# Kernel optimization log

Measured on AMD Instinct MI355X. Metric: run time of the kernel, lower is better.

The kernel has to match this reference:

```python
import jax, jax.numpy as jnp
import numpy as np
from functools import partial

TAU = 2.0       # membrane time constant
V_TH = 1.0      # firing threshold
SLOPE = 10.0    # surrogate sigmoid slope (matches rate_encode's 10*)
T = 10          # time_window
H = 12          # num_heads


def lif_step(v, I):
    """One LIF update: leaky integrate, surrogate spike, multiplicative reset."""
    v = v + (I - v) / TAU
    spk = jax.nn.sigmoid(SLOPE * (v - V_TH))
    v = v * (1.0 - spk)
    return spk, v


def setup_inputs() -> dict:
    key = jax.random.key(0)
    ks = jax.random.split(key, 5)
    B, S, E = 8, 1024, 768
    scale = 1.0 / np.sqrt(E)
    x = jax.random.uniform(ks[0], (B, S, E), dtype=jnp.float32)
    Wq = jax.random.normal(ks[1], (E, E), dtype=jnp.float32) * scale
    Wk = jax.random.normal(ks[2], (E, E), dtype=jnp.float32) * scale
    Wv = jax.random.normal(ks[3], (E, E), dtype=jnp.float32) * scale
    Wo = jax.random.normal(ks[4], (E, E), dtype=jnp.float32) * scale
    zb = jnp.zeros((E,), dtype=jnp.float32)
    return {"x": x, "Wq": Wq, "bq": zb, "Wk": Wk, "bk": zb,
            "Wv": Wv, "bv": zb, "Wo": Wo, "bo": zb}


def reference(x, Wq, bq, Wk, bk, Wv, bv, Wo, bo):
    B, S, E = x.shape
    D = E // H
    # rate encoding probability (x assumed in [0,1] range, clipped)
    p = jnp.clip(x, 0.0, 1.0)  # [B,S,E]

    def step(carry, t):
        vq, vk, vv, Qa, Ka, Va = carry
        inp = jax.nn.sigmoid(SLOPE * (p * T - t))  # [B,S,E] spikes at step t
        qs, vq = lif_step(vq, inp @ Wq.T + bq)
        ks, vk = lif_step(vk, inp @ Wk.T + bk)
        vs, vv = lif_step(vv, inp @ Wv.T + bv)
        return (vq, vk, vv, Qa + qs, Ka + ks, Va + vs), None

    z = jnp.zeros((B, S, E), dtype=x.dtype)
    t_idx = jnp.arange(T, dtype=x.dtype)
    (vq, vk, vv, Q, K, V), _ = jax.lax.scan(step, (z, z, z, z, z, z), t_idx)

    # split heads: [B,S,E] -> [B,H,S,D]
    Qh = Q.reshape(B, S, H, D)
    Kh = K.reshape(B, S, H, D)
    Vh = V.reshape(B, S, H, D)
    scores = jnp.einsum('bqhd,bkhd->bhqk', Qh, Kh) / np.sqrt(D)
    attn = jax.nn.softmax(scores, axis=-1)
    out_h = jnp.einsum('bhqk,bkhd->bqhd', attn, Vh)  # [B,S,H,D]
    out = out_h.reshape(B, S, E)
    # output LIF projection with fresh (zero) state
    out_spk, _ = lif_step(jnp.zeros_like(out), out @ Wo.T + bo)
    return out_spk
```

## Files before the change

### kernel.cpp

```cpp
#include <hip/hip_runtime.h>
#include <math.h>

constexpr int B_ = 8, S_ = 1024, E_ = 768, H_ = 12, D_ = 64, T_ = 10;
constexpr int N_ = B_ * S_;
constexpr int NE_ = N_ * E_;
constexpr int WE_ = E_ * E_;

typedef __attribute__((ext_vector_type(8))) short bf16x8;
typedef __attribute__((ext_vector_type(4))) float f32x4;

#define MFMA16(a,b,c) __builtin_amdgcn_mfma_f32_16x16x32_bf16(a,b,c,0,0,0)

__device__ __forceinline__ float sigm(float z){ return 1.f/(1.f+__expf(-z)); }
__device__ __forceinline__ unsigned short f2bf(float f){
    unsigned int u = __float_as_uint(f);
    u += 0x7FFFu + ((u>>16)&1u);
    return (unsigned short)(u>>16);
}
__device__ __forceinline__ float bf2f(unsigned short h){
    return __uint_as_float(((unsigned int)h)<<16);
}
__device__ __forceinline__ void gl16(const void* g, void* l){
    __builtin_amdgcn_global_load_lds((const __attribute__((address_space(1))) unsigned int*)g,
                                     (__attribute__((address_space(3))) unsigned int*)l, 16, 0, 0);
}

__global__ __launch_bounds__(256) void encode_k(const float* __restrict__ x,
                                                unsigned short* __restrict__ enc){
    const int i = blockIdx.x*256 + threadIdx.x;
    const float4 a = ((const float4*)x)[2*i];
    const float4 b = ((const float4*)x)[2*i+1];
    float p[8] = {a.x,a.y,a.z,a.w,b.x,b.y,b.z,b.w};
#pragma unroll
    for (int e=0;e<8;++e) p[e] = 100.f*fminf(fmaxf(p[e],0.f),1.f);
#pragma unroll
    for (int t=0;t<T_;++t){
        unsigned int w[4];
#pragma unroll
        for (int e=0;e<4;++e){
            unsigned short u0 = f2bf(sigm(p[2*e]   - 10.f*(float)t));
            unsigned short u1 = f2bf(sigm(p[2*e+1] - 10.f*(float)t));
            w[e] = (unsigned int)u0 | ((unsigned int)u1<<16);
        }
        ((uint4*)(enc + (long)t*NE_))[i] = make_uint4(w[0],w[1],w[2],w[3]);
    }
}

__global__ __launch_bounds__(256) void wsplit_k(const float* __restrict__ Wq, const float* __restrict__ Wk,
        const float* __restrict__ Wv, const float* __restrict__ Wo,
        unsigned short* __restrict__ whi, unsigned short* __restrict__ wlo){
    int gi = blockIdx.x*256 + threadIdx.x;
    int z = gi / (WE_/8);
    int r = gi % (WE_/8);
    const float* W = z==0?Wq : z==1?Wk : z==2?Wv : Wo;
    const float4 a = ((const float4*)W)[2*r];
    const float4 b = ((const float4*)W)[2*r+1];
    float f[8]={a.x,a.y,a.z,a.w,b.x,b.y,b.z,b.w};
    unsigned int h[4], l[4];
#pragma unroll
    for (int e=0;e<4;++e){
        unsigned short h0=f2bf(f[2*e]),   l0=f2bf(f[2*e]  -bf2f(h0));
        unsigned short h1=f2bf(f[2*e+1]), l1=f2bf(f[2*e+1]-bf2f(h1));
        h[e] = (unsigned)h0 | ((unsigned)h1<<16);
        l[e] = (unsigned)l0 | ((unsigned)l1<<16);
    }
    ((uint4*)(whi + (long)z*WE_))[r] = make_uint4(h[0],h[1],h[2],h[3]);
    ((uint4*)(wlo + (long)z*WE_))[r] = make_uint4(l[0],l[1],l[2],l[3]);
}

__global__ __launch_bounds__(256,2) void qkv_k(const unsigned short* __restrict__ enc,
        const unsigned short* __restrict__ whi,
        const float* __restrict__ bq, const float* __restrict__ bk, const float* __restrict__ bv,
        float* __restrict__ Qf, float* __restrict__ Kf, float* __restrict__ Vf){
    const int z = blockIdx.z;
    const unsigned short* Wh = whi + (long)z*WE_;
    const float* bias = z==0?bq : z==1?bk : bv;
    float* Out = z==0?Qf : z==1?Kf : Vf;
    const int row0 = blockIdx.x*128, col0 = blockIdx.y*64;

    __shared__ unsigned short Ab[3][128*64];
    __shared__ unsigned short Bh[3][64*64];

    const int tid = threadIdx.x, lane = tid&63, wid = tid>>6;
    const int l15 = lane&15, l4 = lane>>4, l7 = lane&7;
    const int wr = wid>>1, wc = wid&1;

    int aSrc[4], bSrc[2];
#pragma unroll
    for (int s=0;s<4;++s){
        int idx = (wid + s*4)*64 + lane;
        int row = idx>>3, ch = idx&7;
        aSrc[s] = (row0+row)*E_ + ((ch ^ (row&7))<<3);
    }
#pragma unroll
    for (int s=0;s<2;++s){
        int idx = (wid + s*4)*64 + lane;
        int row = idx>>3, ch = idx&7;
        bSrc[s] = (col0+row)*E_ + ((ch ^ (row&7))<<3);
    }

    const int aBase = (wr*64 + l15)*128;
    const int bBase = (wc*32 + l15)*128;
    const int sw[2] = { ((l4^l7)<<4), ((((4+l4))^l7)<<4) };

    f32x4 acc[4][2];
    float vm[4][2][4] = {};
    float qa[4][2][4] = {};
    float bn[2];
#pragma unroll
    for (int n=0;n<2;++n) bn[n] = bias[col0 + wc*32 + n*16 + l15];
    asm volatile("" :: "v"(bn[0]), "v"(bn[1]));

    const f32x4 zero4 = {0.f,0.f,0.f,0.f};

#define STAGE(tt, kk2, slot)                                               \
    do {                                                                   \
        const unsigned short* eb_ = enc + (long)(tt)*NE_ + (kk2)*64;       \
        _Pragma("unroll")                                                  \
        for (int s_=0;s_<4;++s_)                                           \
            gl16(eb_ + aSrc[s_], &Ab[slot][(wid+s_*4)*512]);               \
        _Pragma("unroll")                                                  \
        for (int s_=0;s_<2;++s_)                                           \
            gl16(Wh + bSrc[s_] + (kk2)*64, &Bh[slot][(wid+s_*4)*512]);     \
    } while(0)

    STAGE(0, 0, 0);
    STAGE(0, 1, 1);

    for (int t=0;t<T_;++t){
#pragma unroll
        for (int m=0;m<4;++m)
#pragma unroll
            for (int n=0;n<2;++n) acc[m][n] = zero4;
#pragma unroll
        for (int kt=0;kt<12;++kt){
            const int slotC = kt%3;
            const int slotS = (kt+2)%3;
            if (kt < 10){
                STAGE(t, kt+2, slotS);
                asm volatile("s_waitcnt vmcnt(12)" ::: "memory");
            } else if (t < 9){
                STAGE(t+1, kt-10, slotS);
                asm volatile("s_waitcnt vmcnt(12)" ::: "memory");
            } else if (kt == 10){
                asm volatile("s_waitcnt vmcnt(6)" ::: "memory");
            } else {
                asm volatile("s_waitcnt vmcnt(0)" ::: "memory");
            }
            __builtin_amdgcn_s_barrier();
            __builtin_amdgcn_s_setprio(1);
#pragma unroll
            for (int kk=0;kk<2;++kk){
                bf16x8 af[4], fbh[2];
#pragma unroll
                for (int m=0;m<4;++m)
                    af[m] = *(const bf16x8*)((const char*)&Ab[slotC][0] + aBase + m*2048 + sw[kk]);
#pragma unroll
                for (int n=0;n<2;++n)
                    fbh[n] = *(const bf16x8*)((const char*)&Bh[slotC][0] + bBase + n*2048 + sw[kk]);
#pragma unroll
                for (int m=0;m<4;++m)
#pragma unroll
                    for (int n=0;n<2;++n)
                        acc[m][n] = MFMA16(af[m], fbh[n], acc[m][n]);
            }
            __builtin_amdgcn_s_setprio(0);
            __builtin_amdgcn_s_barrier();
        }
#pragma unroll
        for (int m=0;m<4;++m)
#pragma unroll
            for (int n=0;n<2;++n)
#pragma unroll
                for (int j=0;j<4;++j){
                    float I = acc[m][n][j] + bn[n];
                    float v = (vm[m][n][j] + I)*0.5f;
                    float s = sigm(10.f*v - 10.f);
                    vm[m][n][j] = v*(1.f - s);
                    qa[m][n][j] += s;
                }
    }
#undef STAGE
#pragma unroll
    for (int m=0;m<4;++m)
#pragma unroll
        for (int n=0;n<2;++n)
#pragma unroll
            for (int j=0;j<4;++j){
                int row = row0 + wr*64 + m*16 + l4*4 + j;
                int col = col0 + wc*32 + n*16 + l15;
                Out[(long)row*E_ + col] = qa[m][n][j];
            }
}

__global__ __launch_bounds__(256,2) void attn_k2(const float* __restrict__ Qf, const float* __restrict__ Kf,
        const float* __restrict__ Vf, unsigned short* __restrict__ atth, unsigned short* __restrict__ attl){
    const int q0 = blockIdx.x*64;
    const int h  = blockIdx.y;
    const int b  = blockIdx.z;
    const long base = ((long)b*S_)*E_ + h*64;

    __shared__ char smem[65536];
    unsigned short* Qh = (unsigned short*)(smem);
    unsigned short* Ql = (unsigned short*)(smem + 8192);
    unsigned short* Kh = (unsigned short*)(smem + 16384);
    unsigned short* Kl = (unsigned short*)(smem + 24576);
    unsigned short* Vh = (unsigned short*)(smem + 32768);
    unsigned short* Vl = (unsigned short*)(smem + 40960);
    unsigned short* Ph = (unsigned short*)(smem + 49152);
    unsigned short* Pl = (unsigned short*)(smem + 57344);
    float* OT = (float*)(smem + 16384);

    const int tid = threadIdx.x, lane = tid&63, wid = tid>>6;
    const int l15 = lane&15, l4 = lane>>4, l7 = lane&7;
    const int qrow = wid*16 + l15;

    {
        int q = tid>>2, c0 = (tid&3)*2;
        const float* src = Qf + base + (long)(q0+q)*E_ + (tid&3)*16;
        float4 f0=((const float4*)src)[0], f1=((const float4*)src)[1];
        float4 f2=((const float4*)src)[2], f3=((const float4*)src)[3];
        float f[16]={f0.x,f0.y,f0.z,f0.w,f1.x,f1.y,f1.z,f1.w,f2.x,f2.y,f2.z,f2.w,f3.x,f3.y,f3.z,f3.w};
        bf16x8 vh[2], vl[2];
#pragma unroll
        for (int g=0;g<2;++g)
#pragma unroll
            for (int e=0;e<8;++e){
                unsigned short hh = f2bf(f[g*8+e]);
                vh[g][e] = (short)hh;
                vl[g][e] = (short)f2bf(f[g*8+e]-bf2f(hh));
            }
        int by0 = q*128 + (((c0  ) ^ (q&7))<<4);
        int by1 = q*128 + (((c0+1) ^ (q&7))<<4);
        *(bf16x8*)((char*)Qh + by0) = vh[0];
        *(bf16x8*)((char*)Qh + by1) = vh[1];
        *(bf16x8*)((char*)Ql + by0) = vl[0];
        *(bf16x8*)((char*)Ql + by1) = vl[1];
    }
    __syncthreads();
    bf16x8 qfh[2], qfl[2];
#pragma unroll
    for (int kk=0;kk<2;++kk){
        int off = qrow*128 + ((((kk<<2)+l4) ^ l7)<<4);
        qfh[kk] = *(const bf16x8*)((const char*)Qh + off);
        qfl[kk] = *(const bf16x8*)((const char*)Ql + off);
    }

    float mrun = -1e30f, lrun = 0.f;
    f32x4 ot[4];
    const f32x4 zero4 = {0.f,0.f,0.f,0.f};
#pragma unroll
    for (int m=0;m<4;++m) ot[m] = zero4;

    for (int kt=0;kt<16;++kt){
        const int k0 = kt*64;
        __syncthreads();
        {
            int key = tid>>2, c0 = (tid&3)*2;
            const float* src = Kf + base + (long)(k0+key)*E_ + (tid&3)*16;
            float4 f0=((const float4*)src)[0], f1=((const float4*)src)[1];
            float4 f2=((const float4*)src)[2], f3=((const float4*)src)[3];
            float f[16]={f0.x,f0.y,f0.z,f0.w,f1.x,f1.y,f1.z,f1.w,f2.x,f2.y,f2.z,f2.w,f3.x,f3.y,f3.z,f3.w};
            bf16x8 vh[2], vl[2];
#pragma unroll
            for (int g=0;g<2;++g)
#pragma unroll
                for (int e=0;e<8;++e){
                    unsigned short hh = f2bf(f[g*8+e]);
                    vh[g][e] = (short)hh;
                    vl[g][e] = (short)f2bf(f[g*8+e]-bf2f(hh));
                }
            int by0 = key*128 + (((c0  ) ^ (key&7))<<4);
            int by1 = key*128 + (((c0+1) ^ (key&7))<<4);
            *(bf16x8*)((char*)Kh + by0) = vh[0];
            *(bf16x8*)((char*)Kh + by1) = vh[1];
            *(bf16x8*)((char*)Kl + by0) = vl[0];
            *(bf16x8*)((char*)Kl + by1) = vl[1];
        }
#pragma unroll
        for (int rr=0;rr<2;++rr){
            int dq = (tid>>5) + rr*8;
            int kp = tid&31;
            const float* s0 = Vf + base + (long)(k0 + 2*kp)*E_ + dq*4;
            float4 va = *(const float4*)s0;
            float4 vb = *(const float4*)(s0 + E_);
            float fa[4]={va.x,va.y,va.z,va.w}, fb[4]={vb.x,vb.y,vb.z,vb.w};
#pragma unroll
            for (int dd=0;dd<4;++dd){
                int d = dq*4+dd;
                unsigned short ha=f2bf(fa[dd]), hb=f2bf(fb[dd]);
                unsigned short la=f2bf(fa[dd]-bf2f(ha)), lb=f2bf(fb[dd]-bf2f(hb));
                int byte = d*128 + ((kp<<2) ^ ((d&7)<<4));
                *(unsigned int*)((char*)Vh + byte) = (unsigned)ha | ((unsigned)hb<<16);
                *(unsigned int*)((char*)Vl + byte) = (unsigned)la | ((unsigned)lb<<16);
            }
        }
        __syncthreads();
        f32x4 st[4];
#pragma unroll
        for (int m=0;m<4;++m) st[m] = zero4;
#pragma unroll
        for (int kk=0;kk<2;++kk){
            int swo = ((((kk<<2)+l4) ^ l7)<<4);
            bf16x8 kh[4], kl2[4];
#pragma unroll
            for (int m=0;m<4;++m){
                int off = (m*16+l15)*128 + swo;
                kh[m]  = *(const bf16x8*)((const char*)Kh + off);
                kl2[m] = *(const bf16x8*)((const char*)Kl + off);
            }
#pragma unroll
            for (int m=0;m<4;++m){
                st[m] = MFMA16(kh[m],  qfh[kk], st[m]);
                st[m] = MFMA16(kh[m],  qfl[kk], st[m]);
                st[m] = MFMA16(kl2[m], qfh[kk], st[m]);
            }
        }
        float pmax = -1e30f;
#pragma unroll
        for (int m=0;m<4;++m)
#pragma unroll
            for (int j=0;j<4;++j){ st[m][j] *= 0.125f; pmax = fmaxf(pmax, st[m][j]); }
        pmax = fmaxf(pmax, __shfl_xor(pmax,16));
        pmax = fmaxf(pmax, __shfl_xor(pmax,32));
        float mnew = fmaxf(mrun, pmax);
        float alpha = __expf(mrun - mnew);
        float p[16]; float psum = 0.f;
#pragma unroll
        for (int m=0;m<4;++m)
#pragma unroll
            for (int j=0;j<4;++j){ float e = __expf(st[m][j]-mnew); p[m*4+j]=e; psum+=e; }
        psum += __shfl_xor(psum,16);
        psum += __shfl_xor(psum,32);
        lrun = lrun*alpha + psum;
        mrun = mnew;
#pragma unroll
        for (int m=0;m<4;++m)
#pragma unroll
            for (int j=0;j<4;++j) ot[m][j] *= alpha;
#pragma unroll
        for (int m=0;m<4;++m)
#pragma unroll
            for (int jp=0;jp<2;++jp){
                float fx = p[m*4+jp*2], fy = p[m*4+jp*2+1];
                unsigned short hx=f2bf(fx), hy=f2bf(fy);
                unsigned short lx=f2bf(fx-bf2f(hx)), ly=f2bf(fy-bf2f(hy));
                int key = m*16 + l4*4 + jp*2;
                int byte = qrow*128 + ((key<<1) ^ (l7<<4));
                *(unsigned int*)((char*)Ph + byte) = (unsigned)hx | ((unsigned)hy<<16);
                *(unsigned int*)((char*)Pl + byte) = (unsigned)lx | ((unsigned)ly<<16);
            }
#pragma unroll
        for (int kk=0;kk<2;++kk){
            int swo = ((((kk<<2)+l4) ^ l7)<<4);
            bf16x8 pfh = *(const bf16x8*)((const char*)Ph + qrow*128 + swo);
            bf16x8 pfl = *(const bf16x8*)((const char*)Pl + qrow*128 + swo);
#pragma unroll
            for (int m=0;m<4;++m){
                int off = (m*16+l15)*128 + swo;
                bf16x8 vvh = *(const bf16x8*)((const char*)Vh + off);
                bf16x8 vvl = *(const bf16x8*)((const char*)Vl + off);
                ot[m] = MFMA16(vvh, pfh, ot[m]);
                ot[m] = MFMA16(vvh, pfl, ot[m]);
                ot[m] = MFMA16(vvl, pfh, ot[m]);
            }
        }
    }
    __syncthreads();
    float inv = 1.f/lrun;
#pragma unroll
    for (int m=0;m<4;++m)
#pragma unroll
        for (int j=0;j<4;++j){
            int d = m*16 + l4*4 + j;
            OT[qrow*68 + d] = ot[m][j]*inv;
        }
    __syncthreads();
    {
        int q = tid>>2, d0 = (tid&3)*16;
        const float* rp = OT + q*68 + d0;
        float4 f0=((const float4*)rp)[0], f1=((const float4*)rp)[1];
        float4 f2=((const float4*)rp)[2], f3=((const float4*)rp)[3];
        float f[16]={f0.x,f0.y,f0.z,f0.w,f1.x,f1.y,f1.z,f1.w,f2.x,f2.y,f2.z,f2.w,f3.x,f3.y,f3.z,f3.w};
        bf16x8 vh[2], vl[2];
#pragma unroll
        for (int g=0;g<2;++g)
#pragma unroll
            for (int e=0;e<8;++e){
                unsigned short hh = f2bf(f[g*8+e]);
                vh[g][e] = (short)hh;
                vl[g][e] = (short)f2bf(f[g*8+e]-bf2f(hh));
            }
        long o = base + (long)(q0+q)*E_ + d0;
        *(bf16x8*)(atth + o)     = vh[0];
        *(bf16x8*)(atth + o + 8) = vh[1];
        *(bf16x8*)(attl + o)     = vl[0];
        *(bf16x8*)(attl + o + 8) = vl[1];
    }
}

__global__ __launch_bounds__(256,2) void out_k(const unsigned short* __restrict__ Ah_g,
        const unsigned short* __restrict__ Al_g,
        const unsigned short* __restrict__ Wh, const unsigned short* __restrict__ Wl,
        const float* __restrict__ bias, float* __restrict__ out){
    const int row0 = blockIdx.x*128, col0 = blockIdx.y*64;
    __shared__ unsigned short Ah[128*64], Al[128*64];
    __shared__ unsigned short Bh2[64*64], Bl2[64*64];

    const int tid = threadIdx.x, lane = tid&63, wid = tid>>6;
    const int l15 = lane&15, l4 = lane>>4, l7 = lane&7;
    const int wr = wid>>1, wc = wid&1;

    int aSrc[4], bSrc[2];
#pragma unroll
    for (int s=0;s<4;++s){
        int idx = (wid + s*4)*64 + lane;
        int row = idx>>3, ch = idx&7;
        aSrc[s] = (row0+row)*E_ + ((ch ^ (row&7))<<3);
    }
#pragma unroll
    for (int s=0;s<2;++s){
        int idx = (wid + s*4)*64 + lane;
        int row = idx>>3, ch = idx&7;
        bSrc[s] = (col0+row)*E_ + ((ch ^ (row&7))<<3);
    }
    const int aBase = (wr*64 + l15)*128;
    const int bBase = (wc*32 + l15)*128;
    const int sw[2] = { ((l4^l7)<<4), ((((4+l4))^l7)<<4) };

    f32x4 acc[4][2];
    const f32x4 zero4 = {0.f,0.f,0.f,0.f};
#pragma unroll
    for (int m=0;m<4;++m)
#pragma unroll
        for (int n=0;n<2;++n) acc[m][n] = zero4;

    for (int kt=0;kt<12;++kt){
        const int k0 = kt*64;
        __syncthreads();
#pragma unroll
        for (int s=0;s<4;++s){
            gl16(Ah_g + aSrc[s] + k0, &Ah[(wid+s*4)*512]);
            gl16(Al_g + aSrc[s] + k0, &Al[(wid+s*4)*512]);
        }
#pragma unroll
        for (int s=0;s<2;++s){
            gl16(Wh + bSrc[s] + k0, &Bh2[(wid+s*4)*512]);
            gl16(Wl + bSrc[s] + k0, &Bl2[(wid+s*4)*512]);
        }
        __syncthreads();
#pragma unroll
        for (int kk=0;kk<2;++kk){
            bf16x8 ah[4], al[4], fbh[2], fbl[2];
#pragma unroll
            for (int m=0;m<4;++m){
                ah[m] = *(const bf16x8*)((const char*)Ah + aBase + m*2048 + sw[kk]);
                al[m] = *(const bf16x8*)((const char*)Al + aBase + m*2048 + sw[kk]);
            }
#pragma unroll
            for (int n=0;n<2;++n){
                fbh[n] = *(const bf16x8*)((const char*)Bh2 + bBase + n*2048 + sw[kk]);
                fbl[n] = *(const bf16x8*)((const char*)Bl2 + bBase + n*2048 + sw[kk]);
            }
#pragma unroll
            for (int m=0;m<4;++m)
#pragma unroll
                for (int n=0;n<2;++n){
                    acc[m][n] = MFMA16(ah[m], fbh[n], acc[m][n]);
                    acc[m][n] = MFMA16(ah[m], fbl[n], acc[m][n]);
                    acc[m][n] = MFMA16(al[m], fbh[n], acc[m][n]);
                }
        }
    }
#pragma unroll
    for (int m=0;m<4;++m)
#pragma unroll
        for (int n=0;n<2;++n){
            float bn = bias[col0 + wc*32 + n*16 + l15];
#pragma unroll
            for (int j=0;j<4;++j){
                int row = row0 + wr*64 + m*16 + l4*4 + j;
                int col = col0 + wc*32 + n*16 + l15;
                float I = acc[m][n][j] + bn;
                out[(long)row*E_ + col] = sigm(5.f*I - 10.f);
            }
        }
}

extern "C" void kernel_launch(void* const* d_in, const int* in_sizes, int n_in,
                              void* d_out, int out_size, void* d_ws, size_t ws_size,
                              hipStream_t stream){
    const float* x  = (const float*)d_in[0];
    const float* Wq = (const float*)d_in[1];
    const float* bq = (const float*)d_in[2];
    const float* Wk = (const float*)d_in[3];
    const float* bk = (const float*)d_in[4];
    const float* Wv = (const float*)d_in[5];
    const float* bv = (const float*)d_in[6];
    const float* Wo = (const float*)d_in[7];
    const float* bo = (const float*)d_in[8];
    float* out = (float*)d_out;

    char* ws = (char*)d_ws;
    unsigned short* enc  = (unsigned short*)ws;
    unsigned short* atth = (unsigned short*)ws;
    unsigned short* attl = (unsigned short*)(ws + (long)NE_*2);
    unsigned short* whi  = (unsigned short*)(ws + 125829120L);
    unsigned short* wlo  = whi + 4L*WE_;
    float* Qf = (float*)(ws + 135266304L);
    float* Kf = Qf + NE_;
    float* Vf = Kf + NE_;

    wsplit_k<<<dim3(4*(WE_/8)/256), 256, 0, stream>>>(Wq,Wk,Wv,Wo,whi,wlo);
    encode_k<<<dim3(NE_/8/256), 256, 0, stream>>>(x,enc);
    qkv_k<<<dim3(64,12,3), 256, 0, stream>>>(enc,whi,bq,bk,bv,Qf,Kf,Vf);
    attn_k2<<<dim3(16,12,8), 256, 0, stream>>>(Qf,Kf,Vf,atth,attl);
    out_k<<<dim3(64,12), 256, 0, stream>>>(atth,attl,whi+3L*WE_,wlo+3L*WE_,bo,out);
}
```

Before: 685.4 us.

## Remap QKV and attention blocks per XCD and cut QKV LDS to double buffering

The QKV projection and attention kernels now use a flat 1D grid. Block indices are remapped so each of the 8 XCDs handles a contiguous group of row tiles, or a group of (batch, head) pairs, which is meant to improve L2 reuse of shared operands. The QKV kernel drops from triple to double LDS buffering and raises the launch bound to 3 blocks per CU, trading prefetch depth for occupancy. The shallower pipeline may expose more load latency per k-step.

After: 717.1 us. +4.6%, slower.

```diff
diff --git a/kernel.cpp b/kernel.cpp
--- a/kernel.cpp
+++ b/kernel.cpp
@@ -68,18 +68,24 @@
     ((uint4*)(wlo + (long)z*WE_))[r] = make_uint4(l[0],l[1],l[2],l[3]);
 }
 
-__global__ __launch_bounds__(256,2) void qkv_k(const unsigned short* __restrict__ enc,
+__global__ __launch_bounds__(256,3) void qkv_k(const unsigned short* __restrict__ enc,
         const unsigned short* __restrict__ whi,
         const float* __restrict__ bq, const float* __restrict__ bk, const float* __restrict__ bv,
         float* __restrict__ Qf, float* __restrict__ Kf, float* __restrict__ Vf){
-    const int z = blockIdx.z;
+    const int bid = blockIdx.x;
+    const int xcd = bid & 7;
+    const int vb  = bid >> 3;
+    const int rt  = xcd*8 + (vb & 7);
+    const int yz  = vb >> 3;
+    const int ct  = yz % 12;
+    const int z   = yz / 12;
     const unsigned short* Wh = whi + (long)z*WE_;
     const float* bias = z==0?bq : z==1?bk : bv;
     float* Out = z==0?Qf : z==1?Kf : Vf;
-    const int row0 = blockIdx.x*128, col0 = blockIdx.y*64;
-
-    __shared__ unsigned short Ab[3][128*64];
-    __shared__ unsigned short Bh[3][64*64];
+    const int row0 = rt*128, col0 = ct*64;
+
+    __shared__ unsigned short Ab[2][128*64];
+    __shared__ unsigned short Bh[2][64*64];
 
     const int tid = threadIdx.x, lane = tid&63, wid = tid>>6;
     const int l15 = lane&15, l4 = lane>>4, l7 = lane&7;
@@ -125,7 +131,6 @@
     } while(0)
 
     STAGE(0, 0, 0);
-    STAGE(0, 1, 1);
 
     for (int t=0;t<T_;++t){
 #pragma unroll
@@ -134,15 +139,13 @@
             for (int n=0;n<2;++n) acc[m][n] = zero4;
 #pragma unroll
         for (int kt=0;kt<12;++kt){
-            const int slotC = kt%3;
-            const int slotS = (kt+2)%3;
-            if (kt < 10){
-                STAGE(t, kt+2, slotS);
-                asm volatile("s_waitcnt vmcnt(12)" ::: "memory");
+            const int slotC = kt&1;
+            const int slotS = slotC^1;
+            if (kt < 11){
+                STAGE(t, kt+1, slotS);
+                asm volatile("s_waitcnt vmcnt(6)" ::: "memory");
             } else if (t < 9){
-                STAGE(t+1, kt-10, slotS);
-                asm volatile("s_waitcnt vmcnt(12)" ::: "memory");
-            } else if (kt == 10){
+                STAGE(t+1, 0, slotS);
                 asm volatile("s_waitcnt vmcnt(6)" ::: "memory");
             } else {
                 asm volatile("s_waitcnt vmcnt(0)" ::: "memory");
@@ -195,9 +198,13 @@
 
 __global__ __launch_bounds__(256,2) void attn_k2(const float* __restrict__ Qf, const float* __restrict__ Kf,
         const float* __restrict__ Vf, unsigned short* __restrict__ atth, unsigned short* __restrict__ attl){
-    const int q0 = blockIdx.x*64;
-    const int h  = blockIdx.y;
-    const int b  = blockIdx.z;
+    const int bid = blockIdx.x;
+    const int xcd = bid & 7;
+    const int vb  = bid >> 3;
+    const int q0  = (vb & 15) * 64;
+    const int bhg = xcd*12 + (vb >> 4);
+    const int h   = bhg % 12;
+    const int b   = bhg / 12;
     const long base = ((long)b*S_)*E_ + h*64;
 
     __shared__ char smem[65536];
@@ -513,7 +520,7 @@
 
     wsplit_k<<<dim3(4*(WE_/8)/256), 256, 0, stream>>>(Wq,Wk,Wv,Wo,whi,wlo);
     encode_k<<<dim3(NE_/8/256), 256, 0, stream>>>(x,enc);
-    qkv_k<<<dim3(64,12,3), 256, 0, stream>>>(enc,whi,bq,bk,bv,Qf,Kf,Vf);
-    attn_k2<<<dim3(16,12,8), 256, 0, stream>>>(Qf,Kf,Vf,atth,attl);
+    qkv_k<<<dim3(2304), 256, 0, stream>>>(enc,whi,bq,bk,bv,Qf,Kf,Vf);
+    attn_k2<<<dim3(1536), 256, 0, stream>>>(Qf,Kf,Vf,atth,attl);
     out_k<<<dim3(64,12), 256, 0, stream>>>(atth,attl,whi+3L*WE_,wlo+3L*WE_,bo,out);
 }
```

## Process two timesteps per K-loop pass to reuse weight tiles in QKV kernel

Applied to the files above, without the earlier changes.

The QKV LIF kernel now computes two timesteps together. Each staged weight tile is shared by two encoded-input tiles, with two accumulator sets, so weight loads and barrier count per timestep are halved. The pipeline changes from triple to double buffering to keep LDS usage similar. The cost is twice the accumulator registers, which may hurt occupancy under launch_bounds(256,2), and a shallower prefetch depth.

New measurement: 632.6 us. 7.7% less time.

```diff
diff --git a/kernel.cpp b/kernel.cpp
--- a/kernel.cpp
+++ b/kernel.cpp
@@ -78,8 +78,8 @@
     float* Out = z==0?Qf : z==1?Kf : Vf;
     const int row0 = blockIdx.x*128, col0 = blockIdx.y*64;
 
-    __shared__ unsigned short Ab[3][128*64];
-    __shared__ unsigned short Bh[3][64*64];
+    __shared__ unsigned short Ab[2][2][128*64];
+    __shared__ unsigned short Bh[2][64*64];
 
     const int tid = threadIdx.x, lane = tid&63, wid = tid>>6;
     const int l15 = lane&15, l4 = lane>>4, l7 = lane&7;
@@ -103,7 +103,7 @@
     const int bBase = (wc*32 + l15)*128;
     const int sw[2] = { ((l4^l7)<<4), ((((4+l4))^l7)<<4) };
 
-    f32x4 acc[4][2];
+    f32x4 acc0[4][2], acc1[4][2];
     float vm[4][2][4] = {};
     float qa[4][2][4] = {};
     float bn[2];
@@ -113,37 +113,37 @@
 
     const f32x4 zero4 = {0.f,0.f,0.f,0.f};
 
-#define STAGE(tt, kk2, slot)                                               \
+#define STAGE(tp_, kk2, slot)                                              \
     do {                                                                   \
-        const unsigned short* eb_ = enc + (long)(tt)*NE_ + (kk2)*64;       \
+        const unsigned short* e0_ = enc + (long)(2*(tp_))*NE_ + (kk2)*64;  \
+        const unsigned short* e1_ = e0_ + NE_;                             \
         _Pragma("unroll")                                                  \
-        for (int s_=0;s_<4;++s_)                                           \
-            gl16(eb_ + aSrc[s_], &Ab[slot][(wid+s_*4)*512]);               \
+        for (int s_=0;s_<4;++s_){                                          \
+            gl16(e0_ + aSrc[s_], &Ab[slot][0][(wid+s_*4)*512]);            \
+            gl16(e1_ + aSrc[s_], &Ab[slot][1][(wid+s_*4)*512]);            \
+        }                                                                  \
         _Pragma("unroll")                                                  \
         for (int s_=0;s_<2;++s_)                                           \
             gl16(Wh + bSrc[s_] + (kk2)*64, &Bh[slot][(wid+s_*4)*512]);     \
     } while(0)
 
     STAGE(0, 0, 0);
-    STAGE(0, 1, 1);
-
-    for (int t=0;t<T_;++t){
+
+    for (int tp=0;tp<5;++tp){
 #pragma unroll
         for (int m=0;m<4;++m)
 #pragma unroll
-            for (int n=0;n<2;++n) acc[m][n] = zero4;
+            for (int n=0;n<2;++n){ acc0[m][n] = zero4; acc1[m][n] = zero4; }
 #pragma unroll
         for (int kt=0;kt<12;++kt){
-            const int slotC = kt%3;
-            const int slotS = (kt+2)%3;
-            if (kt < 10){
-                STAGE(t, kt+2, slotS);
-                asm volatile("s_waitcnt vmcnt(12)" ::: "memory");
-            } else if (t < 9){
-                STAGE(t+1, kt-10, slotS);
-                asm volatile("s_waitcnt vmcnt(12)" ::: "memory");
-            } else if (kt == 10){
-                asm volatile("s_waitcnt vmcnt(6)" ::: "memory");
+            const int slotC = kt&1;
+            const int slotS = slotC^1;
+            if (kt < 11){
+                STAGE(tp, kt+1, slotS);
+                asm volatile("s_waitcnt vmcnt(10)" ::: "memory");
+            } else if (tp < 4){
+                STAGE(tp+1, 0, slotS);
+                asm volatile("s_waitcnt vmcnt(10)" ::: "memory");
             } else {
                 asm volatile("s_waitcnt vmcnt(0)" ::: "memory");
             }
@@ -151,18 +151,22 @@
             __builtin_amdgcn_s_setprio(1);
 #pragma unroll
             for (int kk=0;kk<2;++kk){
-                bf16x8 af[4], fbh[2];
-#pragma unroll
-                for (int m=0;m<4;++m)
-                    af[m] = *(const bf16x8*)((const char*)&Ab[slotC][0] + aBase + m*2048 + sw[kk]);
+                bf16x8 af0[4], af1[4], fbh[2];
+#pragma unroll
+                for (int m=0;m<4;++m){
+                    af0[m] = *(const bf16x8*)((const char*)&Ab[slotC][0][0] + aBase + m*2048 + sw[kk]);
+                    af1[m] = *(const bf16x8*)((const char*)&Ab[slotC][1][0] + aBase + m*2048 + sw[kk]);
+                }
 #pragma unroll
                 for (int n=0;n<2;++n)
                     fbh[n] = *(const bf16x8*)((const char*)&Bh[slotC][0] + bBase + n*2048 + sw[kk]);
 #pragma unroll
                 for (int m=0;m<4;++m)
 #pragma unroll
-                    for (int n=0;n<2;++n)
-                        acc[m][n] = MFMA16(af[m], fbh[n], acc[m][n]);
+                    for (int n=0;n<2;++n){
+                        acc0[m][n] = MFMA16(af0[m], fbh[n], acc0[m][n]);
+                        acc1[m][n] = MFMA16(af1[m], fbh[n], acc1[m][n]);
+                    }
             }
             __builtin_amdgcn_s_setprio(0);
             __builtin_amdgcn_s_barrier();
@@ -173,9 +177,14 @@
             for (int n=0;n<2;++n)
 #pragma unroll
                 for (int j=0;j<4;++j){
-                    float I = acc[m][n][j] + bn[n];
-                    float v = (vm[m][n][j] + I)*0.5f;
+                    float I0 = acc0[m][n][j] + bn[n];
+                    float v = (vm[m][n][j] + I0)*0.5f;
                     float s = sigm(10.f*v - 10.f);
+                    v = v*(1.f - s);
+                    qa[m][n][j] += s;
+                    float I1 = acc1[m][n][j] + bn[n];
+                    v = (v + I1)*0.5f;
+                    s = sigm(10.f*v - 10.f);
                     vm[m][n][j] = v*(1.f - s);
                     qa[m][n][j] += s;
                 }
```
